# Performance work log

Hardware: AMD Instinct MI355X
Metric: run time of the kernel (lower is better)

Reference implementation:

```python
import jax, jax.numpy as jnp
import numpy as np

B, I, O = 2048, 512, 512

def setup_inputs() -> dict:
    key = jax.random.key(0)
    kx, kw, ks = jax.random.split(key, 3)
    x = jax.random.uniform(kx, (B, I), dtype=jnp.float32)
    # shift weight logits so sigmoid(w) ~ 0.02: keeps the length-I product
    # of implication factors away from underflow (sparse conjunction)
    w_logits = jax.random.normal(kw, (I, O), dtype=jnp.float32) - 4.0
    s_logits = jax.random.normal(ks, (I, O), dtype=jnp.float32)
    return {"x": x, "w_logits": w_logits, "s_logits": s_logits}

def reference(x, w_logits, s_logits):
    # FuzzyParam.value(): sigmoid of stored logits
    w = jax.nn.sigmoid(w_logits)   # (I, O)
    s = jax.nn.sigmoid(s_logits)   # (I, O)
    xi = x[:, :, None]             # (B, I, 1)
    # product fuzzy logic:
    #   bin_xnor(a, b) = a*b + (1-a)*(1-b)
    #   implies(a, b)  = 1 - a*(1 - b)
    #   conjoin        = prod along axis
    xnor = xi * s + (1.0 - xi) * (1.0 - s)      # (B, I, O)
    factors = 1.0 - w * (1.0 - xnor)            # (B, I, O)
    return jnp.prod(factors, axis=1)            # (B, O)
```

## Files before the change

### kernel.cpp

```cpp
#include <hip/hip_runtime.h>
#include <hip/hip_bf16.h>
#include <math.h>

#define B_DIM 2048
#define I_DIM 512
#define O_DIM 512

constexpr int R_ROWS  = 16;
constexpr int W_CHUNK = 4;
constexpr int CHUNK   = I_DIM / W_CHUNK;
constexpr int KP      = CHUNK / 2;

__global__ __launch_bounds__(256) void precompute_ab(
    const float* __restrict__ w_logits,
    const float* __restrict__ s_logits,
    float4* __restrict__ ab4)
{
    int t = blockIdx.x * 256 + threadIdx.x;
    int o  = t & (O_DIM - 1);
    int k  = t >> 9;
    int i0 = 2 * k;

    float zw0 = w_logits[(i0 + 0) * O_DIM + o];
    float zs0 = s_logits[(i0 + 0) * O_DIM + o];
    float zw1 = w_logits[(i0 + 1) * O_DIM + o];
    float zs1 = s_logits[(i0 + 1) * O_DIM + o];

    float w0 = 1.0f / (1.0f + expf(-zw0));
    float s0 = 1.0f / (1.0f + expf(-zs0));
    float w1 = 1.0f / (1.0f + expf(-zw1));
    float s1 = 1.0f / (1.0f + expf(-zs1));

    float4 v;
    v.x = fmaf(-w0, s0, 1.0f);
    v.y = w0 * (2.0f * s0 - 1.0f);
    v.z = fmaf(-w1, s1, 1.0f);
    v.w = w1 * (2.0f * s1 - 1.0f);
    ab4[k * O_DIM + o] = v;
}

__global__ __launch_bounds__(1024, 4) void fuzzy_main(
    const float* __restrict__ x,
    const float4* __restrict__ ab4,
    float* __restrict__ out)
{
    __shared__ float part[W_CHUNK][8][256];

    const int o_l = threadIdx.x;
    const int o   = blockIdx.x * 256 + o_l;
    const int y   = __builtin_amdgcn_readfirstlane((int)threadIdx.y);
    const int b0  = blockIdx.y * R_ROWS;

    const float*  xp  = x + b0 * I_DIM + y * CHUNK;
    const float4* abp = ab4 + (size_t)(y * KP) * O_DIM + o;

    float acc[R_ROWS];
#pragma unroll
    for (int r = 0; r < R_ROWS; ++r) acc[r] = 1.0f;

    float4 p0 = abp[0];
    float4 p1 = abp[O_DIM];

    for (int k = 0; k < KP; k += 2) {
        float4 c0 = p0;
        float4 c1 = p1;
        p0 = abp[(size_t)(k + 2) * O_DIM];
        p1 = abp[(size_t)(k + 3) * O_DIM];

        const int i = 2 * k;
#pragma unroll
        for (int r = 0; r < R_ROWS; ++r) {
            float x0 = xp[r * I_DIM + i + 0];
            float x1 = xp[r * I_DIM + i + 1];
            float x2 = xp[r * I_DIM + i + 2];
            float x3 = xp[r * I_DIM + i + 3];
            float f0 = fmaf(c0.y, x0, c0.x);
            float f1 = fmaf(c0.w, x1, c0.z);
            float f2 = fmaf(c1.y, x2, c1.x);
            float f3 = fmaf(c1.w, x3, c1.z);
            acc[r] = (acc[r] * (f0 * f1)) * (f2 * f3);
        }
    }

#pragma unroll
    for (int half = 0; half < 2; ++half) {
        if (half) __syncthreads();
#pragma unroll
        for (int rr = 0; rr < 8; ++rr)
            part[y][rr][o_l] = acc[half * 8 + rr];
        __syncthreads();
#pragma unroll
        for (int rr2 = 0; rr2 < 2; ++rr2) {
            int r8 = y * 2 + rr2;
            float v = part[0][r8][o_l] * part[1][r8][o_l]
                    * part[2][r8][o_l] * part[3][r8][o_l];
            out[(size_t)(b0 + half * 8 + r8) * O_DIM + o] = v;
        }
    }
}

extern "C" void kernel_launch(void* const* d_in, const int* in_sizes, int n_in,
                              void* d_out, int out_size, void* d_ws, size_t ws_size,
                              hipStream_t stream) {
    const float* x        = (const float*)d_in[0];
    const float* w_logits = (const float*)d_in[1];
    const float* s_logits = (const float*)d_in[2];
    float* out = (float*)d_out;
    float4* ab4 = (float4*)d_ws;

    precompute_ab<<<dim3((I_DIM / 2) * O_DIM / 256), dim3(256), 0, stream>>>(
        w_logits, s_logits, ab4);

    fuzzy_main<<<dim3(O_DIM / 256, B_DIM / R_ROWS), dim3(256, W_CHUNK), 0, stream>>>(
        x, ab4, out);
}
```

Before: 100.2 us.

## Halve rows per block, split accumulators, and reorder ab4 packing

Cuts rows per block from 16 to 8 and raises the launch-bounds occupancy hint from 4 to 8 blocks, so more blocks and waves are resident to hide latency. Each row now keeps two independent accumulators, which shortens the serial multiply dependency chain. The float4 coefficient packing is reordered, and the prefetch index now wraps with a mask so the last iteration no longer reads past the buffer. The trade-off is that each ab4 load is reused across fewer rows, so coefficient traffic per output rises, and the tighter register budget may cause spills.

```diff
diff --git a/kernel.cpp b/kernel.cpp
--- a/kernel.cpp
+++ b/kernel.cpp
@@ -6,10 +6,11 @@
 #define I_DIM 512
 #define O_DIM 512
 
-constexpr int R_ROWS  = 16;
+constexpr int R_ROWS  = 8;
 constexpr int W_CHUNK = 4;
 constexpr int CHUNK   = I_DIM / W_CHUNK;
 constexpr int KP      = CHUNK / 2;
+constexpr int KROWS   = I_DIM / 2;
 
 __global__ __launch_bounds__(256) void precompute_ab(
     const float* __restrict__ w_logits,
@@ -33,18 +34,18 @@
 
     float4 v;
     v.x = fmaf(-w0, s0, 1.0f);
-    v.y = w0 * (2.0f * s0 - 1.0f);
-    v.z = fmaf(-w1, s1, 1.0f);
+    v.y = fmaf(-w1, s1, 1.0f);
+    v.z = w0 * (2.0f * s0 - 1.0f);
     v.w = w1 * (2.0f * s1 - 1.0f);
     ab4[k * O_DIM + o] = v;
 }
 
-__global__ __launch_bounds__(1024, 4) void fuzzy_main(
+__global__ __launch_bounds__(1024, 8) void fuzzy_main(
     const float* __restrict__ x,
     const float4* __restrict__ ab4,
     float* __restrict__ out)
 {
-    __shared__ float part[W_CHUNK][8][256];
+    __shared__ float part[W_CHUNK][R_ROWS][256];
 
     const int o_l = threadIdx.x;
     const int o   = blockIdx.x * 256 + o_l;
@@ -52,50 +53,51 @@
     const int b0  = blockIdx.y * R_ROWS;
 
     const float*  xp  = x + b0 * I_DIM + y * CHUNK;
-    const float4* abp = ab4 + (size_t)(y * KP) * O_DIM + o;
+    const int     kbase = y * KP;
 
-    float acc[R_ROWS];
+    float acc0[R_ROWS], acc1[R_ROWS];
 #pragma unroll
-    for (int r = 0; r < R_ROWS; ++r) acc[r] = 1.0f;
+    for (int r = 0; r < R_ROWS; ++r) { acc0[r] = 1.0f; acc1[r] = 1.0f; }
 
-    float4 p0 = abp[0];
-    float4 p1 = abp[O_DIM];
+    float4 p0 = ab4[(size_t)(kbase + 0) * O_DIM + o];
+    float4 p1 = ab4[(size_t)(kbase + 1) * O_DIM + o];
 
     for (int k = 0; k < KP; k += 2) {
         float4 c0 = p0;
         float4 c1 = p1;
-        p0 = abp[(size_t)(k + 2) * O_DIM];
-        p1 = abp[(size_t)(k + 3) * O_DIM];
+        int kn = (kbase + k + 2) & (KROWS - 1);
+        p0 = ab4[(size_t)(kn + 0) * O_DIM + o];
+        p1 = ab4[(size_t)(kn + 1) * O_DIM + o];
 
         const int i = 2 * k;
 #pragma unroll
         for (int r = 0; r < R_ROWS; ++r) {
-            float x0 = xp[r * I_DIM + i + 0];
-            float x1 = xp[r * I_DIM + i + 1];
-            float x2 = xp[r * I_DIM + i + 2];
-            float x3 = xp[r * I_DIM + i + 3];
-            float f0 = fmaf(c0.y, x0, c0.x);
-            float f1 = fmaf(c0.w, x1, c0.z);
-            float f2 = fmaf(c1.y, x2, c1.x);
-            float f3 = fmaf(c1.w, x3, c1.z);
-            acc[r] = (acc[r] * (f0 * f1)) * (f2 * f3);
+            const float* xr = xp + r * I_DIM + i;
+            float x0 = xr[0];
+            float x1 = xr[1];
+            float x2 = xr[2];
+            float x3 = xr[3];
+            float f0 = fmaf(c0.z, x0, c0.x);
+            float f1 = fmaf(c0.w, x1, c0.y);
+            float f2 = fmaf(c1.z, x2, c1.x);
+            float f3 = fmaf(c1.w, x3, c1.y);
+            float h0 = f0 * f2;
+            float h1 = f1 * f3;
+            acc0[r] *= h0;
+            acc1[r] *= h1;
         }
     }
 
 #pragma unroll
-    for (int half = 0; half < 2; ++half) {
-        if (half) __syncthreads();
+    for (int r = 0; r < R_ROWS; ++r)
+        part[y][r][o_l] = acc0[r] * acc1[r];
+    __syncthreads();
 #pragma unroll
-        for (int rr = 0; rr < 8; ++rr)
-            part[y][rr][o_l] = acc[half * 8 + rr];
-        __syncthreads();
-#pragma unroll
-        for (int rr2 = 0; rr2 < 2; ++rr2) {
-            int r8 = y * 2 + rr2;
-            float v = part[0][r8][o_l] * part[1][r8][o_l]
-                    * part[2][r8][o_l] * part[3][r8][o_l];
-            out[(size_t)(b0 + half * 8 + r8) * O_DIM + o] = v;
-        }
+    for (int rr = 0; rr < 2; ++rr) {
+        int r8 = y * 2 + rr;
+        float v = part[0][r8][o_l] * part[1][r8][o_l]
+                * part[2][r8][o_l] * part[3][r8][o_l];
+        out[(size_t)(b0 + r8) * O_DIM + o] = v;
     }
 }
 
```

Measured after the change: 94.40 us. -5.8%, faster.
